# Kernel tuning notes

Measured on AMD Instinct MI355X. Metric: run time of the kernel, lower is better.

Reference implementation:

```python
import jax, jax.numpy as jnp
import numpy as np

BN_EPS = 1e-3  # Keras BatchNormalization default epsilon


def _conv_block(x, k):
    """Per-task conv (stride 2, pad 1) -> ReLU -> BatchNorm (center/scale=False, training).

    x: [B, E, H, W, Cin]  (B tasks, E examples per task)
    k: [B, kh, kw, Cin, Cout]  per-task kernel
    """
    def conv_one(xe, kt):  # xe: [E,H,W,Cin], kt: [kh,kw,Cin,Cout]
        return jax.lax.conv_general_dilated(
            xe, kt, window_strides=(2, 2), padding=[(1, 1), (1, 1)],
            dimension_numbers=('NHWC', 'HWIO', 'NHWC'))
    y = jax.nn.relu(jax.vmap(conv_one)(x, k))  # [B,E,H',W',Cout]
    # BatchNorm in training mode: moments over all axes except channels
    m = jnp.mean(y, axis=(0, 1, 2, 3))
    v = jnp.var(y, axis=(0, 1, 2, 3))
    return (y - m) * jax.lax.rsqrt(v + BN_EPS)


def setup_inputs() -> dict:
    key = jax.random.key(0)
    ks = jax.random.split(key, 6)
    B, E, H, C, O = 64, 64, 28, 64, 20
    return {
        'x': jax.random.normal(ks[0], (B, E, H, H, 1), dtype=jnp.float32),
        'k1': jax.random.normal(ks[1], (B, 3, 3, 1, C), dtype=jnp.float32) * 0.1,
        'k2': jax.random.normal(ks[2], (B, 3, 3, C, C), dtype=jnp.float32) * 0.05,
        'k3': jax.random.normal(ks[3], (B, 3, 3, C, C), dtype=jnp.float32) * 0.05,
        'k4': jax.random.normal(ks[4], (B, 3, 3, C, C), dtype=jnp.float32) * 0.05,
        'w_ro': jax.random.normal(ks[5], (B, C, O), dtype=jnp.float32) * 0.1,
    }


def reference(x, k1, k2, k3, k4, w_ro):
    h = _conv_block(x, k1)   # [B,E,14,14,C]
    h = _conv_block(h, k2)   # [B,E,7,7,C]
    h = _conv_block(h, k3)   # [B,E,4,4,C]
    h = _conv_block(h, k4)   # [B,E,2,2,C]
    # MaxPooling2D with pool size == full spatial extent -> global spatial max
    feat = jnp.max(h, axis=(2, 3))  # [B,E,C]
    # per-task readout matmul: [B,E,H] x [B,H,O] -> [B,E,O]
    return jnp.einsum('beh,bho->beo', feat, w_ro)
```

## Files before the change

### kernel.cpp

```cpp
#include <hip/hip_runtime.h>

#define BN_EPS 1e-3f

typedef __attribute__((ext_vector_type(8))) short bf16x8;
typedef __attribute__((ext_vector_type(16))) float floatx16;
typedef unsigned short u16;

__device__ __forceinline__ u16 f2bf(float f) {
  unsigned u = __float_as_uint(f);
  u += 0x7fffu + ((u >> 16) & 1u);
  return (u16)(u >> 16);
}
__device__ __forceinline__ float bf2f(u16 h) {
  return __uint_as_float(((unsigned)h) << 16);
}

static constexpr int NSHARD = 64;

__global__ __launch_bounds__(256) void conv1_stats_k(
    const float* __restrict__ x, const float* __restrict__ k1,
    float* __restrict__ statsSh)
{
  __shared__ float xp[30 * 36];
  __shared__ float w1s[576];
  __shared__ float redsum[64], redss[64];

  const int be = blockIdx.x, b = be >> 6, tid = threadIdx.x;

  for (int i = tid; i < 1080; i += 256) xp[i] = 0.f;
  for (int i = tid; i < 576; i += 256) w1s[i] = k1[(size_t)b * 576 + i];
  if (tid < 64) { redsum[tid] = 0.f; redss[tid] = 0.f; }
  __syncthreads();
  for (int i = tid; i < 784; i += 256) {
    const int r = i / 28, c = i - 28 * r;
    xp[(r + 1) * 36 + (c + 1)] = x[(size_t)be * 784 + i];
  }
  __syncthreads();

  const int cg = (tid & 15) * 4, ps = tid >> 4;
  float wreg[4][9];
#pragma unroll
  for (int cc = 0; cc < 4; ++cc)
#pragma unroll
    for (int t = 0; t < 9; ++t) wreg[cc][t] = w1s[t * 64 + cg + cc];

  float sum[4] = {0.f, 0.f, 0.f, 0.f}, ss[4] = {0.f, 0.f, 0.f, 0.f};
  for (int p = ps; p < 196; p += 16) {
    const int iy = p / 14, ix = p - 14 * iy;
    const float* xb = &xp[(2 * iy) * 36 + 2 * ix];
    float xv[9];
#pragma unroll
    for (int ky = 0; ky < 3; ++ky)
#pragma unroll
      for (int kx = 0; kx < 3; ++kx) xv[ky * 3 + kx] = xb[ky * 36 + kx];
#pragma unroll
    for (int cc = 0; cc < 4; ++cc) {
      float a = 0.f;
#pragma unroll
      for (int t = 0; t < 9; ++t) a = fmaf(xv[t], wreg[cc][t], a);
      const float v = fmaxf(a, 0.f);
      sum[cc] += v;
      ss[cc] = fmaf(v, v, ss[cc]);
    }
  }
#pragma unroll
  for (int cc = 0; cc < 4; ++cc) {
    atomicAdd(&redsum[cg + cc], sum[cc]);
    atomicAdd(&redss[cg + cc], ss[cc]);
  }
  __syncthreads();
  if (tid < 64) {
    const int sh = be & (NSHARD - 1);
    atomicAdd(&statsSh[sh * 128 + tid], redsum[tid]);
    atomicAdd(&statsSh[sh * 128 + 64 + tid], redss[tid]);
  }
}

__global__ __launch_bounds__(256) void foldw_k(
    const float* __restrict__ W, const float* __restrict__ statsSh, float invN,
    u16* __restrict__ Wf, float* __restrict__ biasCls)
{
  __shared__ float T[64 * 68];
  __shared__ float P[256];
  __shared__ float s1[64], t1[64];
  __shared__ float tbS[64];

  const int b = blockIdx.x / 3, sg = blockIdx.x % 3;
  const int tid = threadIdx.x;

  {
    const int g = tid >> 7, cidx = tid & 127;
    float acc = 0.f;
    for (int k = 0; k < NSHARD / 2; ++k)
      acc += statsSh[(g * (NSHARD / 2) + k) * 128 + cidx];
    P[tid] = acc;
  }
  __syncthreads();
  if (tid < 64) {
    const float m = (P[tid] + P[tid + 128]) * invN;
    const float var = fmaf(-m, m, (P[64 + tid] + P[192 + tid]) * invN);
    const float s = rsqrtf(var + BN_EPS);
    s1[tid] = s;
    t1[tid] = -m * s;
  }
  __syncthreads();

  const int cin = tid >> 2, q0 = (tid & 3) * 16;
  const int cout = tid >> 2, ci0 = (tid & 3) * 16;
  for (int s = sg * 3; s < sg * 3 + 3; ++s) {
    if (tid < 64) tbS[tid] = 0.f;
    const float* ss = W + ((size_t)b * 9 + s) * 4096;
#pragma unroll
    for (int q = 0; q < 16; q += 4) {
      const float4 v = *(const float4*)(ss + cin * 64 + q0 + q);
      T[(q0 + q + 0) * 68 + cin] = v.x;
      T[(q0 + q + 1) * 68 + cin] = v.y;
      T[(q0 + q + 2) * 68 + cin] = v.z;
      T[(q0 + q + 3) * 68 + cin] = v.w;
    }
    __syncthreads();
    alignas(16) u16 tmp[16];
    float tb = 0.f;
#pragma unroll
    for (int j = 0; j < 16; ++j) {
      const float wv = T[cout * 68 + ci0 + j];
      tmp[j] = f2bf(wv * s1[ci0 + j]);
      tb = fmaf(t1[ci0 + j], wv, tb);
    }
    u16* dst = Wf + ((size_t)b * 9 + s) * 4096 + cout * 64 + ci0;
    *(uint4*)dst       = *(uint4*)&tmp[0];
    *(uint4*)(dst + 8) = *(uint4*)&tmp[8];
    atomicAdd(&tbS[cout], tb);
    __syncthreads();
    if (tid < 64) {
      const int ky = s / 3, kx = s % 3;
      const float tv = tbS[tid];
#pragma unroll
      for (int cls = 0; cls < 9; ++cls) {
        const int ry = cls / 3, rx = cls % 3;
        const bool valid = !((ry == 1 && ky == 0) || (ry == 2 && ky == 2) ||
                             (rx == 1 && kx == 0) || (rx == 2 && kx == 2));
        if (valid) atomicAdd(&biasCls[(size_t)b * 576 + cls * 64 + tid], tv);
      }
    }
    __syncthreads();
  }
}

__global__ __launch_bounds__(256) void cg2f_k(
    const float* __restrict__ x, const float* __restrict__ k1,
    const u16* __restrict__ k2f, const float* __restrict__ biasCls,
    u16* __restrict__ y2, float* __restrict__ statsSh)
{
  __shared__ __align__(16) u16 mapS[197 * 72];
  __shared__ float xp[30 * 36];
  __shared__ float w1s[576];
  __shared__ float biasS[576];
  __shared__ float redsum[64], redss[64];

  const int be = blockIdx.x, b = be >> 6, tid = threadIdx.x;
  const int lane = tid & 63, wave = tid >> 6;

  for (int i = tid; i < 1080; i += 256) xp[i] = 0.f;
  for (int i = tid; i < 576; i += 256) w1s[i] = k1[(size_t)b * 576 + i];
  for (int i = tid; i < 576; i += 256) biasS[i] = biasCls[(size_t)b * 576 + i];
  if (tid < 64) { redsum[tid] = 0.f; redss[tid] = 0.f; }
  if (tid < 8) *(uint4*)&mapS[196 * 72 + tid * 8] = uint4{0, 0, 0, 0};
  __syncthreads();
  for (int i = tid; i < 784; i += 256) {
    const int r = i / 28, c = i - 28 * r;
    xp[(r + 1) * 36 + (c + 1)] = x[(size_t)be * 784 + i];
  }
  __syncthreads();

  {
    const int cg = (tid & 15) * 4, ps = tid >> 4;
    float wreg[4][9];
#pragma unroll
    for (int cc = 0; cc < 4; ++cc)
#pragma unroll
      for (int t = 0; t < 9; ++t) wreg[cc][t] = w1s[t * 64 + cg + cc];

    for (int p = ps; p < 196; p += 16) {
      const int iy = p / 14, ix = p - 14 * iy;
      const float* xb = &xp[(2 * iy) * 36 + 2 * ix];
      float xv[9];
#pragma unroll
      for (int ky = 0; ky < 3; ++ky)
#pragma unroll
        for (int kx = 0; kx < 3; ++kx) xv[ky * 3 + kx] = xb[ky * 36 + kx];
      alignas(8) u16 o[4];
#pragma unroll
      for (int cc = 0; cc < 4; ++cc) {
        float a = 0.f;
#pragma unroll
        for (int t = 0; t < 9; ++t) a = fmaf(xv[t], wreg[cc][t], a);
        o[cc] = f2bf(fmaxf(a, 0.f));
      }
      *(uint2*)&mapS[p * 72 + cg] = *(uint2*)o;
    }
  }
  __syncthreads();

  const int m0 = (wave & 1) * 32, n0 = (wave >> 1) * 32;
  const int l31 = lane & 31, kq = (lane >> 5) * 8;
  const int lrow = m0 + l31;
  const bool rv = lrow < 49;
  const int oy = rv ? lrow / 7 : 0, ox = rv ? lrow % 7 : 0;
  const u16* wbB = k2f + (size_t)b * 9 * 4096 + (n0 + l31) * 64 + kq;

  floatx16 acc;
#pragma unroll
  for (int r = 0; r < 16; ++r) acc[r] = 0.f;

#pragma unroll
  for (int s = 0; s < 9; ++s) {
    const int ky = s / 3, kx = s % 3;
    int pix = 196;
    if (rv) {
      const int iy = 2 * oy - 1 + ky, ix = 2 * ox - 1 + kx;
      if ((unsigned)iy < 14u && (unsigned)ix < 14u) pix = iy * 14 + ix;
    }
    const u16* ap = &mapS[pix * 72 + kq];
    const u16* bp = wbB + s * 4096;
#pragma unroll
    for (int kk = 0; kk < 4; ++kk) {
      bf16x8 a  = *(const bf16x8*)(ap + kk * 16);
      bf16x8 bv = *(const bf16x8*)(bp + kk * 16);
      acc = __builtin_amdgcn_mfma_f32_32x32x16_bf16(a, bv, acc, 0, 0, 0);
    }
  }

  const int col = n0 + l31;
  const int rb = m0 + 4 * (lane >> 5);
  float ls = 0.f, lss = 0.f;
#pragma unroll
  for (int r = 0; r < 16; ++r) {
    const int rw = rb + (r & 3) + 8 * (r >> 2);
    if (rw < 49) {
      const int ooy = rw / 7, oox = rw % 7;
      const int ry = (ooy == 0) ? 1 : 0;
      const int rx = (oox == 0) ? 1 : 0;
      const float v = fmaxf(acc[r] + biasS[(ry * 3 + rx) * 64 + col], 0.f);
      y2[((size_t)be * 49 + rw) * 64 + col] = f2bf(v);
      ls += v;
      lss = fmaf(v, v, lss);
    }
  }
  atomicAdd(&redsum[col], ls);
  atomicAdd(&redss[col], lss);
  __syncthreads();
  if (tid < 64) {
    const int sh = be & (NSHARD - 1);
    atomicAdd(&statsSh[sh * 128 + tid], redsum[tid]);
    atomicAdd(&statsSh[sh * 128 + 64 + tid], redss[tid]);
  }
}

template <int Hin, int Hout, int G>
__device__ __forceinline__ void conv_core(
    const u16* __restrict__ yin, const u16* __restrict__ Wf,
    const float* __restrict__ biasCls, u16* __restrict__ yout,
    float* __restrict__ statsSh, int blk)
{
  constexpr int PPI  = Hout * Hout;
  constexpr int ROWS = G * PPI;
  constexpr int BPT  = 64 / G;
  constexpr int MR   = G * Hin * Hin;
  constexpr int ZR   = MR;

  __shared__ __align__(16) u16 mapS[(MR + 1) * 72];
  __shared__ float biasS[576];
  __shared__ float redsum[64], redss[64];

  const int b = blk / BPT, e0 = (blk % BPT) * G;
  const int tid = threadIdx.x, lane = tid & 63, wave = tid >> 6;

  for (int i = tid; i < 576; i += 256) biasS[i] = biasCls[(size_t)b * 576 + i];
  if (tid < 64) { redsum[tid] = 0.f; redss[tid] = 0.f; }
  if (tid < 8) *(uint4*)&mapS[ZR * 72 + tid * 8] = uint4{0, 0, 0, 0};

  {
    const u16* src = yin + (size_t)(b * 64 + e0) * (Hin * Hin) * 64;
    for (int ch = tid; ch < MR * 8; ch += 256) {
      const int r = ch >> 3, c8 = ch & 7;
      *(uint4*)&mapS[r * 72 + c8 * 8] = *(const uint4*)(src + ch * 8);
    }
  }

  const int m0 = (wave & 1) * 32, n0 = (wave >> 1) * 32;
  const int l31 = lane & 31, kq = (lane >> 5) * 8;
  const int lrow = m0 + l31;
  const bool rv = lrow < ROWS;
  const int img = rv ? lrow / PPI : 0;
  const int pp  = rv ? lrow % PPI : 0;
  const int oy = pp / Hout, ox = pp % Hout;
  const u16* wbB = Wf + (size_t)b * 9 * 4096 + (n0 + l31) * 64 + kq;

  floatx16 acc;
#pragma unroll
  for (int r = 0; r < 16; ++r) acc[r] = 0.f;

  __syncthreads();

#pragma unroll
  for (int s = 0; s < 9; ++s) {
    const int ky = s / 3, kx = s % 3;
    int pix = ZR;
    if (rv) {
      const int iy = 2 * oy - 1 + ky, ix = 2 * ox - 1 + kx;
      if ((unsigned)iy < (unsigned)Hin && (unsigned)ix < (unsigned)Hin)
        pix = img * (Hin * Hin) + iy * Hin + ix;
    }
    const u16* ap = &mapS[pix * 72 + kq];
    const u16* bp = wbB + s * 4096;
#pragma unroll
    for (int kk = 0; kk < 4; ++kk) {
      bf16x8 a  = *(const bf16x8*)(ap + kk * 16);
      bf16x8 bv = *(const bf16x8*)(bp + kk * 16);
      acc = __builtin_amdgcn_mfma_f32_32x32x16_bf16(a, bv, acc, 0, 0, 0);
    }
  }

  const int col = n0 + l31;
  const int rb = m0 + 4 * (lane >> 5);
  float ls = 0.f, lss = 0.f;
#pragma unroll
  for (int r = 0; r < 16; ++r) {
    const int rw = rb + (r & 3) + 8 * (r >> 2);
    if (rw < ROWS) {
      const int re = rw / PPI, pr = rw % PPI;
      const int ooy = pr / Hout, oox = pr % Hout;
      const int ry = (ooy == 0) ? 1 : ((2 * ooy + 1 >= Hin) ? 2 : 0);
      const int rx = (oox == 0) ? 1 : ((2 * oox + 1 >= Hin) ? 2 : 0);
      const float v = fmaxf(acc[r] + biasS[(ry * 3 + rx) * 64 + col], 0.f);
      yout[((size_t)(b * 64 + e0 + re) * PPI + pr) * 64 + col] = f2bf(v);
      ls += v;
      lss = fmaf(v, v, lss);
    }
  }
  atomicAdd(&redsum[col], ls);
  atomicAdd(&redss[col], lss);
  __syncthreads();
  if (tid < 64) {
    const int sh = blk & (NSHARD - 1);
    atomicAdd(&statsSh[sh * 128 + tid], redsum[tid]);
    atomicAdd(&statsSh[sh * 128 + 64 + tid], redss[tid]);
  }
}

__global__ __launch_bounds__(256) void cg3_k(
    const u16* __restrict__ yin, const u16* __restrict__ Wf,
    const float* __restrict__ biasCls, u16* __restrict__ yout,
    float* __restrict__ statsSh) {
  conv_core<7, 4, 4>(yin, Wf, biasCls, yout, statsSh, blockIdx.x);
}
__global__ __launch_bounds__(256) void cg4_k(
    const u16* __restrict__ yin, const u16* __restrict__ Wf,
    const float* __restrict__ biasCls, u16* __restrict__ yout,
    float* __restrict__ statsSh) {
  conv_core<4, 2, 16>(yin, Wf, biasCls, yout, statsSh, blockIdx.x);
}

__global__ __launch_bounds__(256) void readout_k(
    const u16* __restrict__ y4, const float* __restrict__ w_ro,
    const float* __restrict__ statsSh, float invN, float* __restrict__ outp)
{
  __shared__ float wl[64 * 20];
  __shared__ float feat[64 * 64];
  __shared__ float P[256];
  __shared__ float sArr[64], tArr[64];

  const int b = blockIdx.x, tid = threadIdx.x;

  {
    const int g = tid >> 7, cidx = tid & 127;
    float acc = 0.f;
    for (int k = 0; k < NSHARD / 2; ++k)
      acc += statsSh[(g * (NSHARD / 2) + k) * 128 + cidx];
    P[tid] = acc;
  }
  for (int i = tid; i < 1280; i += 256) wl[i] = w_ro[(size_t)b * 1280 + i];
  __syncthreads();
  if (tid < 64) {
    const float m = (P[tid] + P[tid + 128]) * invN;
    const float var = fmaf(-m, m, (P[64 + tid] + P[192 + tid]) * invN);
    const float s = rsqrtf(var + BN_EPS);
    sArr[tid] = s;
    tArr[tid] = -m * s;
  }
  __syncthreads();

  {
    const int e = tid & 63;
    for (int c = tid >> 6; c < 64; c += 4) {
      const u16* p4 = y4 + ((size_t)(b * 64 + e) * 4) * 64 + c;
      const float v = fmaxf(fmaxf(bf2f(p4[0]), bf2f(p4[64])),
                            fmaxf(bf2f(p4[128]), bf2f(p4[192])));
      feat[c * 64 + e] = fmaf(v, sArr[c], tArr[c]);
    }
  }
  __syncthreads();

  const int e = tid >> 2, og = (tid & 3) * 5;
  float acc[5] = {0.f, 0.f, 0.f, 0.f, 0.f};
  for (int c = 0; c < 64; ++c) {
    const float f = feat[c * 64 + e];
#pragma unroll
    for (int j = 0; j < 5; ++j) acc[j] = fmaf(f, wl[c * 20 + og + j], acc[j]);
  }
#pragma unroll
  for (int j = 0; j < 5; ++j)
    outp[((size_t)b * 64 + e) * 20 + og + j] = acc[j];
}

extern "C" void kernel_launch(void* const* d_in, const int* in_sizes, int n_in,
                              void* d_out, int out_size, void* d_ws, size_t ws_size,
                              hipStream_t stream) {
  (void)in_sizes; (void)n_in; (void)out_size; (void)ws_size;
  const float* x   = (const float*)d_in[0];
  const float* k1  = (const float*)d_in[1];
  const float* k2  = (const float*)d_in[2];
  const float* k3  = (const float*)d_in[3];
  const float* k4  = (const float*)d_in[4];
  const float* wro = (const float*)d_in[5];
  float* out = (float*)d_out;
  char* ws = (char*)d_ws;

  float* stats = (float*)ws;
  float* bias2 = (float*)(ws + 131072);
  float* bias3 = bias2 + 36864;
  float* bias4 = bias3 + 36864;
  u16* k2f = (u16*)(ws + 131072 + 442368);
  u16* k3f = k2f + (size_t)2359296;
  u16* k4f = k3f + (size_t)2359296;
  u16* y2 = k4f + (size_t)2359296;
  u16* y3 = y2 + (size_t)12845056;
  u16* y4 = y3 + (size_t)4194304;

  float* st1 = stats;
  float* st2 = stats + 8192;
  float* st3 = stats + 16384;
  float* st4 = stats + 24576;

  hipMemsetAsync(stats, 0, 131072 + 442368, stream);

  conv1_stats_k<<<4096, 256, 0, stream>>>(x, k1, st1);
  foldw_k<<<192, 256, 0, stream>>>(k2, st1, 1.f / 802816.f, k2f, bias2);
  cg2f_k<<<4096, 256, 0, stream>>>(x, k1, k2f, bias2, y2, st2);
  foldw_k<<<192, 256, 0, stream>>>(k3, st2, 1.f / 200704.f, k3f, bias3);
  cg3_k<<<1024, 256, 0, stream>>>(y2, k3f, bias3, y3, st3);
  foldw_k<<<192, 256, 0, stream>>>(k4, st3, 1.f / 65536.f, k4f, bias4);
  cg4_k<<<256, 256, 0, stream>>>(y3, k4f, bias4, y4, st4);
  readout_k<<<64, 256, 0, stream>>>(y4, wro, st4, 1.f / 16384.f, out);
}
```

Baseline: 296.0 us.

## Apply BatchNorm on activation load instead of folding into weights; MFMA conv1

The three per-layer foldw kernels, which scaled the weights by the BN statistics and built per-border-class bias tables, are removed. The BN affine is now applied to the activations as each conv kernel loads them into shared memory, with the statistics reduced inside each consumer block. A single prep kernel transposes and converts all three weight tensors to bf16 up front, which takes weight prep off the serial stats-dependent chain. The first 3x3 single-channel conv now runs on 32x32x16 bf16 MFMA in both the stats pass and the fused conv2 kernel, at the cost of bf16 rounding of the inputs and redundant per-block stats reductions.

```diff
diff --git a/kernel.cpp b/kernel.cpp
--- a/kernel.cpp
+++ b/kernel.cpp
@@ -17,7 +17,41 @@
 
 static constexpr int NSHARD = 64;
 
-__global__ __launch_bounds__(256) void conv1_stats_k(
+__global__ __launch_bounds__(256) void prep_k(
+    const float* __restrict__ k2, const float* __restrict__ k3,
+    const float* __restrict__ k4, u16* __restrict__ k2T,
+    u16* __restrict__ k3T, u16* __restrict__ k4T)
+{
+  __shared__ float T[64 * 68];
+  const int blk = blockIdx.x, l = blk >> 6, b = blk & 63;
+  const float* src = (l == 0 ? k2 : l == 1 ? k3 : k4) + (size_t)b * 9 * 4096;
+  u16* dst = (l == 0 ? k2T : l == 1 ? k3T : k4T) + (size_t)b * 9 * 4096;
+  const int tid = threadIdx.x;
+  const int cin = tid >> 2, q0 = (tid & 3) * 16;
+  const int cout = tid >> 2, ci0 = (tid & 3) * 16;
+
+  for (int s = 0; s < 9; ++s) {
+    const float* ss = src + s * 4096;
+#pragma unroll
+    for (int q = 0; q < 16; q += 4) {
+      const float4 v = *(const float4*)(ss + cin * 64 + q0 + q);
+      T[(q0 + q + 0) * 68 + cin] = v.x;
+      T[(q0 + q + 1) * 68 + cin] = v.y;
+      T[(q0 + q + 2) * 68 + cin] = v.z;
+      T[(q0 + q + 3) * 68 + cin] = v.w;
+    }
+    __syncthreads();
+    alignas(16) u16 tmp[16];
+#pragma unroll
+    for (int j = 0; j < 16; ++j) tmp[j] = f2bf(T[cout * 68 + ci0 + j]);
+    u16* d = dst + s * 4096 + cout * 64 + ci0;
+    *(uint4*)d       = *(uint4*)&tmp[0];
+    *(uint4*)(d + 8) = *(uint4*)&tmp[8];
+    __syncthreads();
+  }
+}
+
+__global__ __launch_bounds__(256) void conv1s_k(
     const float* __restrict__ x, const float* __restrict__ k1,
     float* __restrict__ statsSh)
 {
@@ -26,6 +60,8 @@
   __shared__ float redsum[64], redss[64];
 
   const int be = blockIdx.x, b = be >> 6, tid = threadIdx.x;
+  const int lane = tid & 63, wave = tid >> 6;
+  const int l31 = lane & 31, kq8 = (lane >> 5) * 8;
 
   for (int i = tid; i < 1080; i += 256) xp[i] = 0.f;
   for (int i = tid; i < 576; i += 256) w1s[i] = k1[(size_t)b * 576 + i];
@@ -37,37 +73,47 @@
   }
   __syncthreads();
 
-  const int cg = (tid & 15) * 4, ps = tid >> 4;
-  float wreg[4][9];
-#pragma unroll
-  for (int cc = 0; cc < 4; ++cc)
-#pragma unroll
-    for (int t = 0; t < 9; ++t) wreg[cc][t] = w1s[t * 64 + cg + cc];
-
-  float sum[4] = {0.f, 0.f, 0.f, 0.f}, ss[4] = {0.f, 0.f, 0.f, 0.f};
-  for (int p = ps; p < 196; p += 16) {
-    const int iy = p / 14, ix = p - 14 * iy;
-    const float* xb = &xp[(2 * iy) * 36 + 2 * ix];
-    float xv[9];
-#pragma unroll
-    for (int ky = 0; ky < 3; ++ky)
-#pragma unroll
-      for (int kx = 0; kx < 3; ++kx) xv[ky * 3 + kx] = xb[ky * 36 + kx];
-#pragma unroll
-    for (int cc = 0; cc < 4; ++cc) {
-      float a = 0.f;
-#pragma unroll
-      for (int t = 0; t < 9; ++t) a = fmaf(xv[t], wreg[cc][t], a);
-      const float v = fmaxf(a, 0.f);
-      sum[cc] += v;
-      ss[cc] = fmaf(v, v, ss[cc]);
-    }
-  }
-#pragma unroll
-  for (int cc = 0; cc < 4; ++cc) {
-    atomicAdd(&redsum[cg + cc], sum[cc]);
-    atomicAdd(&redss[cg + cc], ss[cc]);
-  }
+  bf16x8 bf0, bf1;
+#pragma unroll
+  for (int j = 0; j < 8; ++j) {
+    const int k = kq8 + j;
+    bf0[j] = (k < 9) ? (short)f2bf(w1s[k * 64 + l31]) : (short)0;
+    bf1[j] = (k < 9) ? (short)f2bf(w1s[k * 64 + 32 + l31]) : (short)0;
+  }
+
+  float s0 = 0.f, q0 = 0.f, s1v = 0.f, q1 = 0.f;
+  for (int t = wave; t < 7; t += 4) {
+    const int row = t * 32 + l31;
+    const int p = row < 196 ? row : 195;
+    const int oy = p / 14, ox = p - 14 * oy;
+    bf16x8 af;
+#pragma unroll
+    for (int j = 0; j < 8; ++j) {
+      const int k = kq8 + j;
+      float v = 0.f;
+      if (k < 9) v = xp[(2 * oy + k / 3) * 36 + (2 * ox + k % 3)];
+      af[j] = (short)f2bf(v);
+    }
+    floatx16 z;
+#pragma unroll
+    for (int r = 0; r < 16; ++r) z[r] = 0.f;
+    floatx16 c0 = __builtin_amdgcn_mfma_f32_32x32x16_bf16(af, bf0, z, 0, 0, 0);
+    floatx16 c1 = __builtin_amdgcn_mfma_f32_32x32x16_bf16(af, bf1, z, 0, 0, 0);
+    const int rb = t * 32 + 4 * (lane >> 5);
+#pragma unroll
+    for (int r = 0; r < 16; ++r) {
+      const int rw = rb + (r & 3) + 8 * (r >> 2);
+      if (rw < 196) {
+        const float v0 = fmaxf(c0[r], 0.f), v1 = fmaxf(c1[r], 0.f);
+        s0 += v0; q0 = fmaf(v0, v0, q0);
+        s1v += v1; q1 = fmaf(v1, v1, q1);
+      }
+    }
+  }
+  atomicAdd(&redsum[l31], s0);
+  atomicAdd(&redss[l31], q0);
+  atomicAdd(&redsum[32 + l31], s1v);
+  atomicAdd(&redss[32 + l31], q1);
   __syncthreads();
   if (tid < 64) {
     const int sh = be & (NSHARD - 1);
@@ -76,24 +122,32 @@
   }
 }
 
-__global__ __launch_bounds__(256) void foldw_k(
-    const float* __restrict__ W, const float* __restrict__ statsSh, float invN,
-    u16* __restrict__ Wf, float* __restrict__ biasCls)
+__global__ __launch_bounds__(256) void cg2f_k(
+    const float* __restrict__ x, const float* __restrict__ k1,
+    const u16* __restrict__ k2T, const float* __restrict__ statsPrev,
+    float invN, u16* __restrict__ y2, float* __restrict__ statsSh)
 {
-  __shared__ float T[64 * 68];
+  __shared__ __align__(16) u16 mapS[225 * 72];
+  __shared__ float xp[30 * 36];
+  __shared__ float w1s[576];
   __shared__ float P[256];
   __shared__ float s1[64], t1[64];
-  __shared__ float tbS[64];
-
-  const int b = blockIdx.x / 3, sg = blockIdx.x % 3;
-  const int tid = threadIdx.x;
-
-  {
-    const int g = tid >> 7, cidx = tid & 127;
-    float acc = 0.f;
+  __shared__ float redsum[64], redss[64];
+
+  const int be = blockIdx.x, b = be >> 6, tid = threadIdx.x;
+  const int lane = tid & 63, wave = tid >> 6;
+  const int l31 = lane & 31, kq8 = (lane >> 5) * 8;
+
+  for (int i = tid; i < 1080; i += 256) xp[i] = 0.f;
+  for (int i = tid; i < 576; i += 256) w1s[i] = k1[(size_t)b * 576 + i];
+  if (tid < 64) { redsum[tid] = 0.f; redss[tid] = 0.f; }
+  if (tid < 9) *(uint4*)&mapS[224 * 72 + tid * 8] = uint4{0, 0, 0, 0};
+  {
+    const int cidx = tid & 127, g = tid >> 7;
+    float a = 0.f;
     for (int k = 0; k < NSHARD / 2; ++k)
-      acc += statsSh[(g * (NSHARD / 2) + k) * 128 + cidx];
-    P[tid] = acc;
+      a += statsPrev[(g * (NSHARD / 2) + k) * 128 + cidx];
+    P[tid] = a;
   }
   __syncthreads();
   if (tid < 64) {
@@ -103,70 +157,6 @@
     s1[tid] = s;
     t1[tid] = -m * s;
   }
-  __syncthreads();
-
-  const int cin = tid >> 2, q0 = (tid & 3) * 16;
-  const int cout = tid >> 2, ci0 = (tid & 3) * 16;
-  for (int s = sg * 3; s < sg * 3 + 3; ++s) {
-    if (tid < 64) tbS[tid] = 0.f;
-    const float* ss = W + ((size_t)b * 9 + s) * 4096;
-#pragma unroll
-    for (int q = 0; q < 16; q += 4) {
-      const float4 v = *(const float4*)(ss + cin * 64 + q0 + q);
-      T[(q0 + q + 0) * 68 + cin] = v.x;
-      T[(q0 + q + 1) * 68 + cin] = v.y;
-      T[(q0 + q + 2) * 68 + cin] = v.z;
-      T[(q0 + q + 3) * 68 + cin] = v.w;
-    }
-    __syncthreads();
-    alignas(16) u16 tmp[16];
-    float tb = 0.f;
-#pragma unroll
-    for (int j = 0; j < 16; ++j) {
-      const float wv = T[cout * 68 + ci0 + j];
-      tmp[j] = f2bf(wv * s1[ci0 + j]);
-      tb = fmaf(t1[ci0 + j], wv, tb);
-    }
-    u16* dst = Wf + ((size_t)b * 9 + s) * 4096 + cout * 64 + ci0;
-    *(uint4*)dst       = *(uint4*)&tmp[0];
-    *(uint4*)(dst + 8) = *(uint4*)&tmp[8];
-    atomicAdd(&tbS[cout], tb);
-    __syncthreads();
-    if (tid < 64) {
-      const int ky = s / 3, kx = s % 3;
-      const float tv = tbS[tid];
-#pragma unroll
-      for (int cls = 0; cls < 9; ++cls) {
-        const int ry = cls / 3, rx = cls % 3;
-        const bool valid = !((ry == 1 && ky == 0) || (ry == 2 && ky == 2) ||
-                             (rx == 1 && kx == 0) || (rx == 2 && kx == 2));
-        if (valid) atomicAdd(&biasCls[(size_t)b * 576 + cls * 64 + tid], tv);
-      }
-    }
-    __syncthreads();
-  }
-}
-
-__global__ __launch_bounds__(256) void cg2f_k(
-    const float* __restrict__ x, const float* __restrict__ k1,
-    const u16* __restrict__ k2f, const float* __restrict__ biasCls,
-    u16* __restrict__ y2, float* __restrict__ statsSh)
-{
-  __shared__ __align__(16) u16 mapS[197 * 72];
-  __shared__ float xp[30 * 36];
-  __shared__ float w1s[576];
-  __shared__ float biasS[576];
-  __shared__ float redsum[64], redss[64];
-
-  const int be = blockIdx.x, b = be >> 6, tid = threadIdx.x;
-  const int lane = tid & 63, wave = tid >> 6;
-
-  for (int i = tid; i < 1080; i += 256) xp[i] = 0.f;
-  for (int i = tid; i < 576; i += 256) w1s[i] = k1[(size_t)b * 576 + i];
-  for (int i = tid; i < 576; i += 256) biasS[i] = biasCls[(size_t)b * 576 + i];
-  if (tid < 64) { redsum[tid] = 0.f; redss[tid] = 0.f; }
-  if (tid < 8) *(uint4*)&mapS[196 * 72 + tid * 8] = uint4{0, 0, 0, 0};
-  __syncthreads();
   for (int i = tid; i < 784; i += 256) {
     const int r = i / 28, c = i - 28 * r;
     xp[(r + 1) * 36 + (c + 1)] = x[(size_t)be * 784 + i];
@@ -174,40 +164,48 @@
   __syncthreads();
 
   {
-    const int cg = (tid & 15) * 4, ps = tid >> 4;
-    float wreg[4][9];
-#pragma unroll
-    for (int cc = 0; cc < 4; ++cc)
-#pragma unroll
-      for (int t = 0; t < 9; ++t) wreg[cc][t] = w1s[t * 64 + cg + cc];
-
-    for (int p = ps; p < 196; p += 16) {
-      const int iy = p / 14, ix = p - 14 * iy;
-      const float* xb = &xp[(2 * iy) * 36 + 2 * ix];
-      float xv[9];
-#pragma unroll
-      for (int ky = 0; ky < 3; ++ky)
-#pragma unroll
-        for (int kx = 0; kx < 3; ++kx) xv[ky * 3 + kx] = xb[ky * 36 + kx];
-      alignas(8) u16 o[4];
-#pragma unroll
-      for (int cc = 0; cc < 4; ++cc) {
-        float a = 0.f;
-#pragma unroll
-        for (int t = 0; t < 9; ++t) a = fmaf(xv[t], wreg[cc][t], a);
-        o[cc] = f2bf(fmaxf(a, 0.f));
+    bf16x8 bf0, bf1;
+#pragma unroll
+    for (int j = 0; j < 8; ++j) {
+      const int k = kq8 + j;
+      bf0[j] = (k < 9) ? (short)f2bf(w1s[k * 64 + l31]) : (short)0;
+      bf1[j] = (k < 9) ? (short)f2bf(w1s[k * 64 + 32 + l31]) : (short)0;
+    }
+    const float sc0 = s1[l31], tc0 = t1[l31];
+    const float sc1 = s1[32 + l31], tc1 = t1[32 + l31];
+    for (int t = wave; t < 7; t += 4) {
+      const int row = t * 32 + l31;
+      const int p = row < 196 ? row : 195;
+      const int oy = p / 14, ox = p - 14 * oy;
+      bf16x8 af;
+#pragma unroll
+      for (int j = 0; j < 8; ++j) {
+        const int k = kq8 + j;
+        float v = 0.f;
+        if (k < 9) v = xp[(2 * oy + k / 3) * 36 + (2 * ox + k % 3)];
+        af[j] = (short)f2bf(v);
       }
-      *(uint2*)&mapS[p * 72 + cg] = *(uint2*)o;
+      floatx16 z;
+#pragma unroll
+      for (int r = 0; r < 16; ++r) z[r] = 0.f;
+      floatx16 c0 = __builtin_amdgcn_mfma_f32_32x32x16_bf16(af, bf0, z, 0, 0, 0);
+      floatx16 c1 = __builtin_amdgcn_mfma_f32_32x32x16_bf16(af, bf1, z, 0, 0, 0);
+      const int rb = t * 32 + 4 * (lane >> 5);
+#pragma unroll
+      for (int r = 0; r < 16; ++r) {
+        const int rw = rb + (r & 3) + 8 * (r >> 2);
+        mapS[rw * 72 + l31]      = f2bf(fmaf(fmaxf(c0[r], 0.f), sc0, tc0));
+        mapS[rw * 72 + 32 + l31] = f2bf(fmaf(fmaxf(c1[r], 0.f), sc1, tc1));
+      }
     }
   }
   __syncthreads();
 
   const int m0 = (wave & 1) * 32, n0 = (wave >> 1) * 32;
-  const int l31 = lane & 31, kq = (lane >> 5) * 8;
   const int lrow = m0 + l31;
   const bool rv = lrow < 49;
   const int oy = rv ? lrow / 7 : 0, ox = rv ? lrow % 7 : 0;
-  const u16* wbB = k2f + (size_t)b * 9 * 4096 + (n0 + l31) * 64 + kq;
+  const u16* wbB = k2T + (size_t)b * 9 * 4096 + (n0 + l31) * 64 + kq8;
 
   floatx16 acc;
 #pragma unroll
@@ -216,12 +214,12 @@
 #pragma unroll
   for (int s = 0; s < 9; ++s) {
     const int ky = s / 3, kx = s % 3;
-    int pix = 196;
+    int pix = 224;
     if (rv) {
       const int iy = 2 * oy - 1 + ky, ix = 2 * ox - 1 + kx;
       if ((unsigned)iy < 14u && (unsigned)ix < 14u) pix = iy * 14 + ix;
     }
-    const u16* ap = &mapS[pix * 72 + kq];
+    const u16* ap = &mapS[pix * 72 + kq8];
     const u16* bp = wbB + s * 4096;
 #pragma unroll
     for (int kk = 0; kk < 4; ++kk) {
@@ -238,10 +236,7 @@
   for (int r = 0; r < 16; ++r) {
     const int rw = rb + (r & 3) + 8 * (r >> 2);
     if (rw < 49) {
-      const int ooy = rw / 7, oox = rw % 7;
-      const int ry = (ooy == 0) ? 1 : 0;
-      const int rx = (oox == 0) ? 1 : 0;
-      const float v = fmaxf(acc[r] + biasS[(ry * 3 + rx) * 64 + col], 0.f);
+      const float v = fmaxf(acc[r], 0.f);
       y2[((size_t)be * 49 + rw) * 64 + col] = f2bf(v);
       ls += v;
       lss = fmaf(v, v, lss);
@@ -258,9 +253,9 @@
 }
 
 template <int Hin, int Hout, int G>
-__device__ __forceinline__ void conv_core(
-    const u16* __restrict__ yin, const u16* __restrict__ Wf,
-    const float* __restrict__ biasCls, u16* __restrict__ yout,
+__device__ __forceinline__ void conv_core_bn(
+    const u16* __restrict__ yin, const u16* __restrict__ wT,
+    const float* __restrict__ statsPrev, float invN, u16* __restrict__ yout,
     float* __restrict__ statsSh, int blk)
 {
   constexpr int PPI  = Hout * Hout;
@@ -270,32 +265,54 @@
   constexpr int ZR   = MR;
 
   __shared__ __align__(16) u16 mapS[(MR + 1) * 72];
-  __shared__ float biasS[576];
+  __shared__ float P[256];
+  __shared__ float s1[64], t1[64];
   __shared__ float redsum[64], redss[64];
 
   const int b = blk / BPT, e0 = (blk % BPT) * G;
   const int tid = threadIdx.x, lane = tid & 63, wave = tid >> 6;
 
-  for (int i = tid; i < 576; i += 256) biasS[i] = biasCls[(size_t)b * 576 + i];
   if (tid < 64) { redsum[tid] = 0.f; redss[tid] = 0.f; }
-  if (tid < 8) *(uint4*)&mapS[ZR * 72 + tid * 8] = uint4{0, 0, 0, 0};
+  if (tid < 9) *(uint4*)&mapS[ZR * 72 + tid * 8] = uint4{0, 0, 0, 0};
+  {
+    const int cidx = tid & 127, g = tid >> 7;
+    float a = 0.f;
+    for (int k = 0; k < NSHARD / 2; ++k)
+      a += statsPrev[(g * (NSHARD / 2) + k) * 128 + cidx];
+    P[tid] = a;
+  }
+  __syncthreads();
+  if (tid < 64) {
+    const float m = (P[tid] + P[tid + 128]) * invN;
+    const float var = fmaf(-m, m, (P[64 + tid] + P[192 + tid]) * invN);
+    const float s = rsqrtf(var + BN_EPS);
+    s1[tid] = s;
+    t1[tid] = -m * s;
+  }
+  __syncthreads();
 
   {
     const u16* src = yin + (size_t)(b * 64 + e0) * (Hin * Hin) * 64;
     for (int ch = tid; ch < MR * 8; ch += 256) {
-      const int r = ch >> 3, c8 = ch & 7;
-      *(uint4*)&mapS[r * 72 + c8 * 8] = *(const uint4*)(src + ch * 8);
+      const int r = ch >> 3, c0 = (ch & 7) * 8;
+      uint4 v = *(const uint4*)(src + ch * 8);
+      const u16* h = (const u16*)&v;
+      alignas(16) u16 o[8];
+#pragma unroll
+      for (int j = 0; j < 8; ++j)
+        o[j] = f2bf(fmaf(bf2f(h[j]), s1[c0 + j], t1[c0 + j]));
+      *(uint4*)&mapS[r * 72 + c0] = *(uint4*)o;
     }
   }
 
   const int m0 = (wave & 1) * 32, n0 = (wave >> 1) * 32;
-  const int l31 = lane & 31, kq = (lane >> 5) * 8;
+  const int l31 = lane & 31, kq8 = (lane >> 5) * 8;
   const int lrow = m0 + l31;
   const bool rv = lrow < ROWS;
   const int img = rv ? lrow / PPI : 0;
   const int pp  = rv ? lrow % PPI : 0;
   const int oy = pp / Hout, ox = pp % Hout;
-  const u16* wbB = Wf + (size_t)b * 9 * 4096 + (n0 + l31) * 64 + kq;
+  const u16* wbB = wT + (size_t)b * 9 * 4096 + (n0 + l31) * 64 + kq8;
 
   floatx16 acc;
 #pragma unroll
@@ -312,7 +329,7 @@
       if ((unsigned)iy < (unsigned)Hin && (unsigned)ix < (unsigned)Hin)
         pix = img * (Hin * Hin) + iy * Hin + ix;
     }
-    const u16* ap = &mapS[pix * 72 + kq];
+    const u16* ap = &mapS[pix * 72 + kq8];
     const u16* bp = wbB + s * 4096;
 #pragma unroll
     for (int kk = 0; kk < 4; ++kk) {
@@ -330,10 +347,7 @@
     const int rw = rb + (r & 3) + 8 * (r >> 2);
     if (rw < ROWS) {
       const int re = rw / PPI, pr = rw % PPI;
-      const int ooy = pr / Hout, oox = pr % Hout;
-      const int ry = (ooy == 0) ? 1 : ((2 * ooy + 1 >= Hin) ? 2 : 0);
-      const int rx = (oox == 0) ? 1 : ((2 * oox + 1 >= Hin) ? 2 : 0);
-      const float v = fmaxf(acc[r] + biasS[(ry * 3 + rx) * 64 + col], 0.f);
+      const float v = fmaxf(acc[r], 0.f);
       yout[((size_t)(b * 64 + e0 + re) * PPI + pr) * 64 + col] = f2bf(v);
       ls += v;
       lss = fmaf(v, v, lss);
@@ -350,16 +364,16 @@
 }
 
 __global__ __launch_bounds__(256) void cg3_k(
-    const u16* __restrict__ yin, const u16* __restrict__ Wf,
-    const float* __restrict__ biasCls, u16* __restrict__ yout,
+    const u16* __restrict__ yin, const u16* __restrict__ wT,
+    const float* __restrict__ stPrev, float invN, u16* __restrict__ yout,
     float* __restrict__ statsSh) {
-  conv_core<7, 4, 4>(yin, Wf, biasCls, yout, statsSh, blockIdx.x);
+  conv_core_bn<7, 4, 4>(yin, wT, stPrev, invN, yout, statsSh, blockIdx.x);
 }
 __global__ __launch_bounds__(256) void cg4_k(
-    const u16* __restrict__ yin, const u16* __restrict__ Wf,
-    const float* __restrict__ biasCls, u16* __restrict__ yout,
+    const u16* __restrict__ yin, const u16* __restrict__ wT,
+    const float* __restrict__ stPrev, float invN, u16* __restrict__ yout,
     float* __restrict__ statsSh) {
-  conv_core<4, 2, 16>(yin, Wf, biasCls, yout, statsSh, blockIdx.x);
+  conv_core_bn<4, 2, 16>(yin, wT, stPrev, invN, yout, statsSh, blockIdx.x);
 }
 
 __global__ __launch_bounds__(256) void readout_k(
@@ -428,13 +442,10 @@
   char* ws = (char*)d_ws;
 
   float* stats = (float*)ws;
-  float* bias2 = (float*)(ws + 131072);
-  float* bias3 = bias2 + 36864;
-  float* bias4 = bias3 + 36864;
-  u16* k2f = (u16*)(ws + 131072 + 442368);
-  u16* k3f = k2f + (size_t)2359296;
-  u16* k4f = k3f + (size_t)2359296;
-  u16* y2 = k4f + (size_t)2359296;
+  u16* k2T = (u16*)(ws + 131072);
+  u16* k3T = k2T + (size_t)2359296;
+  u16* k4T = k3T + (size_t)2359296;
+  u16* y2 = k4T + (size_t)2359296;
   u16* y3 = y2 + (size_t)12845056;
   u16* y4 = y3 + (size_t)4194304;
 
@@ -443,14 +454,12 @@
   float* st3 = stats + 16384;
   float* st4 = stats + 24576;
 
-  hipMemsetAsync(stats, 0, 131072 + 442368, stream);
-
-  conv1_stats_k<<<4096, 256, 0, stream>>>(x, k1, st1);
-  foldw_k<<<192, 256, 0, stream>>>(k2, st1, 1.f / 802816.f, k2f, bias2);
-  cg2f_k<<<4096, 256, 0, stream>>>(x, k1, k2f, bias2, y2, st2);
-  foldw_k<<<192, 256, 0, stream>>>(k3, st2, 1.f / 200704.f, k3f, bias3);
-  cg3_k<<<1024, 256, 0, stream>>>(y2, k3f, bias3, y3, st3);
-  foldw_k<<<192, 256, 0, stream>>>(k4, st3, 1.f / 65536.f, k4f, bias4);
-  cg4_k<<<256, 256, 0, stream>>>(y3, k4f, bias4, y4, st4);
+  hipMemsetAsync(stats, 0, 131072, stream);
+
+  prep_k<<<192, 256, 0, stream>>>(k2, k3, k4, k2T, k3T, k4T);
+  conv1s_k<<<4096, 256, 0, stream>>>(x, k1, st1);
+  cg2f_k<<<4096, 256, 0, stream>>>(x, k1, k2T, st1, 1.f / 802816.f, y2, st2);
+  cg3_k<<<1024, 256, 0, stream>>>(y2, k3T, st2, 1.f / 200704.f, y3, st3);
+  cg4_k<<<256, 256, 0, stream>>>(y3, k4T, st3, 1.f / 65536.f, y4, st4);
   readout_k<<<64, 256, 0, stream>>>(y4, wro, st4, 1.f / 16384.f, out);
 }
```

After: 275.9 us. 6.8% less time.
